# Kernel optimization log

Hardware: AMD Instinct MI355X
Metric: run time of the kernel (lower is better)

## Reference

```python
import jax, jax.numpy as jnp
import numpy as np

B, T, DI, H, L = 32, 512, 512, 512, 4  # num_layers=4 -> 1 base LSTM + 3 CALSTM layers


def setup_inputs() -> dict:
    key = jax.random.key(0)
    ks = jax.random.split(key, 4)
    s_ih = 1.0 / np.sqrt(DI)
    s_hh = 1.0 / np.sqrt(H)
    s_ca = 1.0 / np.sqrt(2 * H)
    return {
        "x": jax.random.normal(ks[0], (B, T, DI), dtype=jnp.float32),
        "w_ih": jax.random.normal(ks[1], (4 * H, DI), dtype=jnp.float32) * s_ih,
        "w_hh": jax.random.normal(ks[2], (4 * H, H), dtype=jnp.float32) * s_hh,
        "b_ih": jnp.zeros((4 * H,), jnp.float32),
        "b_hh": jnp.zeros((4 * H,), jnp.float32),
        "ca_w": jax.random.normal(ks[3], (L - 1, 5 * H, 2 * H), dtype=jnp.float32) * s_ca,
        "ca_b": jnp.zeros((L - 1, 5 * H), jnp.float32),
    }


def _stacked_lstm(x, w_ih, w_hh, b_ih, b_hh, ca_w, ca_b):
    b = x.shape[0]
    z = jnp.zeros((b, H), x.dtype)
    bias = b_ih + b_hh

    # --- layer 0: StatefulLSTM (plain LSTM cell) ---
    def base_step(carry, x_t):
        h, c = carry
        m = x_t @ w_ih.T + h @ w_hh.T + bias  # (B, 4H)
        i, f, g, o = jnp.split(m, 4, axis=1)
        c = jax.nn.sigmoid(i) * jnp.tanh(g) + jax.nn.sigmoid(f) * c
        h = jax.nn.sigmoid(o) * jnp.tanh(c)
        return (h, c), (h, c)

    _, (hs, cs) = jax.lax.scan(base_step, (z, z), jnp.swapaxes(x, 0, 1))  # (T,B,H) each

    # --- layers 1..L-1: CALSTM with fuse_type='add' ---
    for l in range(ca_w.shape[0]):
        Wl, bl = ca_w[l], ca_b[l]

        def ca_step(carry, xt, Wl=Wl, bl=bl):
            h_prev, c_prev = carry
            h_low, c_low = xt
            m = jnp.concatenate([h_low, h_prev], axis=1) @ Wl.T + bl  # (B, 5H)
            i, f_prev, f_low, u, o = jnp.split(m, 5, axis=1)
            c = (c_prev * jax.nn.sigmoid(f_prev + 1.0)
                 + c_low * jax.nn.sigmoid(f_low + 1.0)
                 + jnp.tanh(u) * jax.nn.sigmoid(i))
            h = jax.nn.sigmoid(o) * jnp.tanh(c)
            return (h, c), (h, c)

        _, (hs, cs) = jax.lax.scan(ca_step, (z, z), (hs, cs))

    hs = jnp.swapaxes(hs, 0, 1)  # (B, T, H)
    cs = jnp.swapaxes(cs, 0, 1)
    return hs, cs


def reference(x, w_ih, w_hh, b_ih, b_hh, ca_w, ca_b):
    hs, cs = _stacked_lstm(x, w_ih, w_hh, b_ih, b_hh, ca_w, ca_b)
    # ((hs, cs), hx) with hx = last step state (length=None path)
    return (hs, cs, hs[:, -1], cs[:, -1])
```

## Files before the change

### kernel.cpp

```cpp
#include <hip/hip_runtime.h>
#include <math.h>


#define TT 512
#define HH 512
#define ROWP 1032
#define W_OFF 0
#define A_OFF 82560
#define RED_OFF A_OFF
#define MF_OFF (A_OFF + 49152)
#define LDS_BYTES (A_OFF + 66048)

#define CWS_OFF 65536
#define FL_OFF  196608
#define WS_ZERO_WORDS (FL_OFF + 1024)

typedef _Float16 half8 __attribute__((ext_vector_type(8)));
typedef float f32x4 __attribute__((ext_vector_type(4)));

__global__ void zero_ws_k(unsigned* __restrict__ ws){
    int i = blockIdx.x*blockDim.x + threadIdx.x;
    for (; i < WS_ZERO_WORDS; i += gridDim.x*blockDim.x) ws[i] = 0u;
}

__device__ __forceinline__ float sigm(float v){ return 1.f/(1.f+__expf(-v)); }

__device__ __forceinline__ void poll_layer(const unsigned* fl, int L, unsigned need){
    const int i = threadIdx.x & 63;
    const unsigned* p = fl + (L*64 + i)*4;
    for (;;){
        const unsigned v = __hip_atomic_load(p, __ATOMIC_RELAXED, __HIP_MEMORY_SCOPE_AGENT);
        if (__all((int)(v >= need))) break;
        __builtin_amdgcn_s_sleep(2);
    }
}

template<int MT>
__device__ void run_loop(const float* __restrict__ x, const float* __restrict__ b_ih,
                         const float* __restrict__ b_hh, const float* __restrict__ ca_b,
                         float* __restrict__ out, float* __restrict__ ws_f,
                         char* lds, int layer, int ub)
{
    const int tid  = threadIdx.x;
    const int lane = tid & 63;
    const int wv   = tid >> 6;
    const int i16  = lane & 15, qq = lane >> 4;
    unsigned short* hws = (unsigned short*)ws_f;
    float*    cws = ws_f + CWS_OFF;
    unsigned* fl  = (unsigned*)ws_f + FL_OFF;

    const int gu = tid & 7, gb = tid >> 3, gj = ub*8 + gu;
    float bias[5] = {0,0,0,0,0};
    if (tid < 256){
        if (MT == 2){
#pragma unroll
            for (int g = 0; g < 4; ++g) bias[g] = b_ih[g*512+gj] + b_hh[g*512+gj];
        } else {
            const float* cbl = ca_b + (layer-1)*2560;
#pragma unroll
            for (int g = 0; g < 5; ++g) bias[g] = cbl[g*512+gj];
            bias[1] += 1.f; bias[2] += 1.f;
        }
    }
    if (tid == 0 && layer > 0)
        __hip_atomic_store(fl + (layer*64+ub)*4, (unsigned)layer,
                           __ATOMIC_RELAXED, __HIP_MEMORY_SCOPE_AGENT);

    for (int tau = layer; tau < TT + layer; ++tau){
        const int t = tau - layer;
        const int p = tau & 1, q = p ^ 1;

        uint4 xpk[8];
        if (MT == 2 && (tid & 127) < 64){
#pragma unroll
            for (int it = 0; it < 8; ++it){
                const int cidx = tid + it*512;
                const int b = cidx >> 7, kc = (cidx & 127) << 3;
                const float* xs = x + ((size_t)b*TT + t)*HH + kc;
                const float4 a = *(const float4*)xs;
                const float4 c = *(const float4*)(xs + 4);
                union { _Float16 h[8]; uint4 u; } pk;
                pk.h[0]=(_Float16)a.x; pk.h[1]=(_Float16)a.y;
                pk.h[2]=(_Float16)a.z; pk.h[3]=(_Float16)a.w;
                pk.h[4]=(_Float16)c.x; pk.h[5]=(_Float16)c.y;
                pk.h[6]=(_Float16)c.z; pk.h[7]=(_Float16)c.w;
                xpk[it] = pk.u;
            }
        }

        if (wv == 0)                    poll_layer(fl, layer,   (unsigned)tau);
        else if (wv == 1 && MT == 3)    poll_layer(fl, layer-1, (unsigned)tau);
        if (wv == 0) __builtin_amdgcn_fence(__ATOMIC_ACQUIRE, "agent");
        __syncthreads();

        float cpv = 0.f, clov = 0.f;
        if (tid < 256){
            cpv = cws[(layer*2+q)*16384 + gb*512 + gj];
            if (MT == 3) clov = cws[((layer-1)*2+q)*16384 + gb*512 + gj];
        }

        if (MT == 2){
            if ((tid & 127) < 64){
#pragma unroll
                for (int it = 0; it < 8; ++it){
                    const int cidx = tid + it*512;
                    const int b = cidx >> 7, kc = (cidx & 127) << 3;
                    *(uint4*)(lds + A_OFF + (size_t)(b*ROWP + kc)*2) = xpk[it];
                }
            } else {
                const unsigned short* hprev = hws + (layer*2+q)*16384;
#pragma unroll
                for (int it = 0; it < 8; ++it){
                    const int cidx = tid + it*512;
                    const int b = cidx >> 7, kc = (cidx & 127) << 3;
                    const uint4 v = *(const uint4*)(hprev + b*512 + (kc - 512));
                    *(uint4*)(lds + A_OFF + (size_t)(b*ROWP + kc)*2) = v;
                }
            }
        } else {
            const unsigned short* hlow  = hws + ((layer-1)*2+q)*16384;
            const unsigned short* hprev = hws + (layer*2+q)*16384;
#pragma unroll
            for (int it = 0; it < 8; ++it){
                const int cidx = tid + it*512;
                const int b = cidx >> 7, kc = (cidx & 127) << 3;
                const uint4 v = (kc < 512) ? *(const uint4*)(hlow  + b*512 + kc)
                                           : *(const uint4*)(hprev + b*512 + (kc - 512));
                *(uint4*)(lds + A_OFF + (size_t)(b*ROWP + kc)*2) = v;
            }
        }
        __syncthreads();

        f32x4 acc[MT][2];
#pragma unroll
        for (int mt = 0; mt < MT; ++mt){ acc[mt][0] = (f32x4){0,0,0,0}; acc[mt][1] = (f32x4){0,0,0,0}; }
#pragma unroll
        for (int s = 0; s < 4; ++s){
            const int koff = wv*128 + s*32 + qq*8;
            half8 bfrag0 = *(const half8*)(lds + A_OFF + ((0*16 + i16)*ROWP + koff)*2);
            half8 bfrag1 = *(const half8*)(lds + A_OFF + ((1*16 + i16)*ROWP + koff)*2);
#pragma unroll
            for (int mt = 0; mt < MT; ++mt){
                half8 afrag = *(const half8*)(lds + W_OFF + ((mt*16 + i16)*ROWP + koff)*2);
                acc[mt][0] = __builtin_amdgcn_mfma_f32_16x16x32_f16(afrag, bfrag0, acc[mt][0], 0, 0, 0);
                acc[mt][1] = __builtin_amdgcn_mfma_f32_16x16x32_f16(afrag, bfrag1, acc[mt][1], 0, 0, 0);
            }
        }
        __syncthreads();

#pragma unroll
        for (int mt = 0; mt < MT; ++mt)
#pragma unroll
            for (int nt = 0; nt < 2; ++nt)
#pragma unroll
                for (int r = 0; r < 4; ++r){
                    const int m = mt*16 + qq*4 + r, n = nt*16 + i16;
                    *(float*)(lds + RED_OFF + ((wv*48 + m)*32 + n)*4) = acc[mt][nt][r];
                }
        __syncthreads();

        const int rows = (MT == 2) ? 32 : 40;
        for (int o = tid; o < rows*32; o += 512){
            const int m = o >> 5, n = o & 31;
            float sm = 0.f;
#pragma unroll
            for (int kq = 0; kq < 8; ++kq)
                sm += *(float*)(lds + RED_OFF + ((kq*48 + m)*32 + n)*4);
            *(float*)(lds + MF_OFF + o*4) = sm;
        }
        __syncthreads();

        float hval = 0.f, cval = 0.f;
        if (tid < 256){
            const float* mf = (const float*)(lds + MF_OFF);
            if (MT == 2){
                const float mi  = mf[(0*8+gu)*32 + gb] + bias[0];
                const float mff = mf[(1*8+gu)*32 + gb] + bias[1];
                const float mg  = mf[(2*8+gu)*32 + gb] + bias[2];
                const float mo  = mf[(3*8+gu)*32 + gb] + bias[3];
                cval = sigm(mi)*tanhf(mg) + sigm(mff)*cpv;
                hval = sigm(mo)*tanhf(cval);
            } else {
                const float mi  = mf[(0*8+gu)*32 + gb] + bias[0];
                const float mfp = mf[(1*8+gu)*32 + gb] + bias[1];
                const float mfl = mf[(2*8+gu)*32 + gb] + bias[2];
                const float mu  = mf[(3*8+gu)*32 + gb] + bias[3];
                const float mo  = mf[(4*8+gu)*32 + gb] + bias[4];
                cval = cpv*sigm(mfp) + clov*sigm(mfl) + tanhf(mu)*sigm(mi);
                hval = sigm(mo)*tanhf(cval);
            }
        }

        if (layer < 3){
            if (wv == 0) poll_layer(fl, layer+1, (unsigned)tau);
            __syncthreads();
        }

        const float hnb = __shfl_down(hval, 1);
        if (tid < 256){
            __hip_atomic_store(&cws[(layer*2+p)*16384 + gb*512 + gj], cval,
                               __ATOMIC_RELAXED, __HIP_MEMORY_SCOPE_AGENT);
            if ((gu & 1) == 0){
                union { _Float16 h2[2]; unsigned u; } pk;
                pk.h2[0] = (_Float16)hval; pk.h2[1] = (_Float16)hnb;
                __hip_atomic_store((unsigned*)(hws + (layer*2+p)*16384 + gb*512 + gj),
                                   pk.u, __ATOMIC_RELAXED, __HIP_MEMORY_SCOPE_AGENT);
            }
        }
        asm volatile("s_waitcnt vmcnt(0)" ::: "memory");
        __syncthreads();
        if (tid == 0)
            __hip_atomic_store(fl + (layer*64+ub)*4, (unsigned)(tau + 1),
                               __ATOMIC_RELAXED, __HIP_MEMORY_SCOPE_AGENT);

        if (layer == 3 && tid < 256){
            const size_t pos = ((size_t)gb*TT + t)*HH + gj;
            out[pos]           = hval;
            out[8388608 + pos] = cval;
            if (t == TT-1){
                out[16777216 + (size_t)gb*HH + gj] = hval;
                out[16793600 + (size_t)gb*HH + gj] = cval;
            }
        }
    }
    if (tid == 0)
        __hip_atomic_store(fl + (layer*64+ub)*4, 0x7FFFFFFFu,
                           __ATOMIC_RELAXED, __HIP_MEMORY_SCOPE_AGENT);
}

__global__ __launch_bounds__(512) void persist_k(
    const float* __restrict__ x, const float* __restrict__ w_ih,
    const float* __restrict__ w_hh, const float* __restrict__ b_ih,
    const float* __restrict__ b_hh, const float* __restrict__ ca_w,
    const float* __restrict__ ca_b, float* __restrict__ out,
    float* __restrict__ ws_f)
{
    extern __shared__ char lds[];
    const int bx = blockIdx.x;
    const int layer = bx >> 6, ub = bx & 63;
    const int tid = threadIdx.x;
    const int rows = (layer == 0) ? 32 : 40;

    for (int idx = tid; idx < rows*256; idx += 512){
        const int r = idx >> 8, k4 = (idx & 255) * 4;
        const int g = r >> 3, u = r & 7;
        const int grow = g*512 + ub*8 + u;
        const float* src;
        if (layer == 0) src = (k4 < 512) ? (w_ih + (size_t)grow*512 + k4)
                                         : (w_hh + (size_t)grow*512 + (k4 - 512));
        else            src = ca_w + (size_t)(layer-1)*2560*1024 + (size_t)grow*1024 + k4;
        const float4 v = *(const float4*)src;
        union { _Float16 h[4]; uint2 u2; } pk;
        pk.h[0]=(_Float16)v.x; pk.h[1]=(_Float16)v.y;
        pk.h[2]=(_Float16)v.z; pk.h[3]=(_Float16)v.w;
        *(uint2*)(lds + W_OFF + ((size_t)(r*ROWP + k4))*2) = pk.u2;
    }
    if (layer == 0) run_loop<2>(x, b_ih, b_hh, ca_b, out, ws_f, lds, layer, ub);
    else            run_loop<3>(x, b_ih, b_hh, ca_b, out, ws_f, lds, layer, ub);
}

extern "C" void kernel_launch(void* const* d_in, const int* in_sizes, int n_in,
                              void* d_out, int out_size, void* d_ws, size_t ws_size,
                              hipStream_t stream)
{
    const float* x    = (const float*)d_in[0];
    const float* w_ih = (const float*)d_in[1];
    const float* w_hh = (const float*)d_in[2];
    const float* b_ih = (const float*)d_in[3];
    const float* b_hh = (const float*)d_in[4];
    const float* ca_w = (const float*)d_in[5];
    const float* ca_b = (const float*)d_in[6];
    float* out = (float*)d_out;
    float* ws  = (float*)d_ws;

    (void)hipFuncSetAttribute((const void*)persist_k,
                              hipFuncAttributeMaxDynamicSharedMemorySize, LDS_BYTES);
    hipLaunchKernelGGL(zero_ws_k, dim3(64), dim3(256), 0, stream, (unsigned*)ws);
    hipLaunchKernelGGL(persist_k, dim3(256), dim3(512), LDS_BYTES, stream,
                       x, w_ih, w_hh, b_ih, b_hh, ca_w, ca_b, out, ws);
}
```

Measured before the change: 3.139 ms.

## Restructure persistent LSTM pipeline with per-wave flags, triple buffering and fragment-ordered weights

Weights are stored in LDS pre-swizzled into MFMA fragment order, and B fragments are loaded straight from global memory into registers, which removes the LDS staging of activations and one barrier. The gate waves keep the cell state in registers and publish per-wave progress flags. Other waves poll only the specific producers they depend on, and a triple-buffered h/c workspace loosens the handshake with the next layer. The risks are more global memory traffic per wave and more complex flag logic that could cause deadlock or race hazards.

```diff
diff --git a/kernel.cpp b/kernel.cpp
--- a/kernel.cpp
+++ b/kernel.cpp
@@ -4,16 +4,12 @@
 
 #define TT 512
 #define HH 512
-#define ROWP 1032
-#define W_OFF 0
-#define A_OFF 82560
-#define RED_OFF A_OFF
-#define MF_OFF (A_OFF + 49152)
-#define LDS_BYTES (A_OFF + 66048)
-
-#define CWS_OFF 65536
-#define FL_OFF  196608
-#define WS_ZERO_WORDS (FL_OFF + 1024)
+
+#define CWS_OFF 98304
+#define FL_OFF  294912
+#define WS_ZERO_WORDS 299008
+
+#define LDS_BYTES 147456
 
 typedef _Float16 half8 __attribute__((ext_vector_type(8)));
 typedef float f32x4 __attribute__((ext_vector_type(4)));
@@ -25,19 +21,15 @@
 
 __device__ __forceinline__ float sigm(float v){ return 1.f/(1.f+__expf(-v)); }
 
-__device__ __forceinline__ void poll_layer(const unsigned* fl, int L, unsigned need){
-    const int i = threadIdx.x & 63;
-    const unsigned* p = fl + (L*64 + i)*4;
-    for (;;){
-        const unsigned v = __hip_atomic_load(p, __ATOMIC_RELAXED, __HIP_MEMORY_SCOPE_AGENT);
-        if (__all((int)(v >= need))) break;
-        __builtin_amdgcn_s_sleep(2);
-    }
+__device__ __forceinline__ unsigned fload(const unsigned* p){
+    return __hip_atomic_load(p, __ATOMIC_RELAXED, __HIP_MEMORY_SCOPE_AGENT);
 }
 
 template<int MT>
-__device__ void run_loop(const float* __restrict__ x, const float* __restrict__ b_ih,
-                         const float* __restrict__ b_hh, const float* __restrict__ ca_b,
+__device__ void run_loop(const float* __restrict__ x,
+                         const float* __restrict__ w_ih, const float* __restrict__ w_hh,
+                         const float* __restrict__ b_ih, const float* __restrict__ b_hh,
+                         const float* __restrict__ ca_w, const float* __restrict__ ca_b,
                          float* __restrict__ out, float* __restrict__ ws_f,
                          char* lds, int layer, int ub)
 {
@@ -45,13 +37,42 @@
     const int lane = tid & 63;
     const int wv   = tid >> 6;
     const int i16  = lane & 15, qq = lane >> 4;
+    const bool isGate = (wv >= 4);
     unsigned short* hws = (unsigned short*)ws_f;
     float*    cws = ws_f + CWS_OFF;
     unsigned* fl  = (unsigned*)ws_f + FL_OFF;
-
-    const int gu = tid & 7, gb = tid >> 3, gj = ub*8 + gu;
+    float* red = (float*)(lds + MT*32768);
+
+    for (int idx = tid; idx < MT*2048; idx += 512){
+        const int ll  = idx & 63;
+        const int s   = (idx >> 6) & 3;
+        const int wvv = (idx >> 8) & 7;
+        const int mt  = idx >> 11;
+        const int r   = mt*16 + (ll & 15);
+        const int k   = wvv*128 + s*32 + (ll >> 4)*8;
+        union { _Float16 h[8]; uint4 u; } pk;
+        if (MT == 3 && r >= 40){
+            pk.u = make_uint4(0u,0u,0u,0u);
+        } else {
+            const int g = r >> 3, u = r & 7;
+            const int grow = g*512 + ub*8 + u;
+            const float* src;
+            if (MT == 2) src = (k < 512) ? (w_ih + (size_t)grow*512 + k)
+                                         : (w_hh + (size_t)grow*512 + (k - 512));
+            else         src = ca_w + (size_t)(layer-1)*2560*1024 + (size_t)grow*1024 + k;
+            const float4 a = *(const float4*)src;
+            const float4 b = *(const float4*)(src + 4);
+            pk.h[0]=(_Float16)a.x; pk.h[1]=(_Float16)a.y; pk.h[2]=(_Float16)a.z; pk.h[3]=(_Float16)a.w;
+            pk.h[4]=(_Float16)b.x; pk.h[5]=(_Float16)b.y; pk.h[6]=(_Float16)b.z; pk.h[7]=(_Float16)b.w;
+        }
+        *(uint4*)(lds + idx*16) = pk.u;
+    }
+
+    const int gtid = tid - 256;
+    const int gu = gtid & 7, gbl = gtid >> 3;
+    const int gj = ub*8 + gu;
     float bias[5] = {0,0,0,0,0};
-    if (tid < 256){
+    if (isGate){
         if (MT == 2){
 #pragma unroll
             for (int g = 0; g < 4; ++g) bias[g] = b_ih[g*512+gj] + b_hh[g*512+gj];
@@ -62,170 +83,178 @@
             bias[1] += 1.f; bias[2] += 1.f;
         }
     }
-    if (tid == 0 && layer > 0)
-        __hip_atomic_store(fl + (layer*64+ub)*4, (unsigned)layer,
+
+    const unsigned* pollp  = nullptr;
+    const unsigned* belowp = nullptr;
+    const unsigned* warp_p = nullptr;
+    if (isGate){
+        pollp = fl + ((layer*64 + ((wv-4)*16 + (lane>>2)))*4 + (lane&3))*4;
+        if (MT == 3) belowp = fl + (((layer-1)*64 + ub)*4 + (wv-4))*4;
+    } else if (MT == 3){
+        pollp = fl + (((layer-1)*64 + (wv*16 + (lane>>2)))*4 + (lane&3))*4;
+    }
+    if (wv == 0 && layer < 3) warp_p = fl + (((layer+1)*64 + lane)*4 + 0)*4;
+
+    if (tid < 4)
+        __hip_atomic_store(fl + ((layer*64+ub)*4 + tid)*4, (unsigned)layer,
                            __ATOMIC_RELAXED, __HIP_MEMORY_SCOPE_AGENT);
+    __syncthreads();
+
+    float creg = 0.f;
 
     for (int tau = layer; tau < TT + layer; ++tau){
-        const int t = tau - layer;
-        const int p = tau & 1, q = p ^ 1;
-
-        uint4 xpk[8];
-        if (MT == 2 && (tid & 127) < 64){
-#pragma unroll
-            for (int it = 0; it < 8; ++it){
-                const int cidx = tid + it*512;
-                const int b = cidx >> 7, kc = (cidx & 127) << 3;
-                const float* xs = x + ((size_t)b*TT + t)*HH + kc;
-                const float4 a = *(const float4*)xs;
-                const float4 c = *(const float4*)(xs + 4);
-                union { _Float16 h[8]; uint4 u; } pk;
-                pk.h[0]=(_Float16)a.x; pk.h[1]=(_Float16)a.y;
-                pk.h[2]=(_Float16)a.z; pk.h[3]=(_Float16)a.w;
-                pk.h[4]=(_Float16)c.x; pk.h[5]=(_Float16)c.y;
-                pk.h[6]=(_Float16)c.z; pk.h[7]=(_Float16)c.w;
-                xpk[it] = pk.u;
-            }
-        }
-
-        if (wv == 0)                    poll_layer(fl, layer,   (unsigned)tau);
-        else if (wv == 1 && MT == 3)    poll_layer(fl, layer-1, (unsigned)tau);
-        if (wv == 0) __builtin_amdgcn_fence(__ATOMIC_ACQUIRE, "agent");
+        const int t  = tau - layer;
+        const int pb = tau % 3;
+        const int qb = (tau + 2) % 3;
+
+        if (warp_p){
+            const unsigned need = (tau >= 1) ? (unsigned)(tau - 1) : 0u;
+            for (;;){
+                if (__all((int)(fload(warp_p) >= need))) break;
+                __builtin_amdgcn_s_sleep(1);
+            }
+        }
+
+        if (MT == 3 && !isGate){
+            for (;;){
+                if (__all((int)(fload(pollp) >= (unsigned)tau))) break;
+                __builtin_amdgcn_s_sleep(1);
+            }
+            __builtin_amdgcn_fence(__ATOMIC_ACQUIRE, "agent");
+        }
+        if (isGate){
+            if (MT == 3){
+                for (;;){
+                    const unsigned v1 = fload(pollp);
+                    const unsigned v2 = fload(belowp);
+                    if (__all((int)(v1 >= (unsigned)tau && v2 >= (unsigned)tau))) break;
+                    __builtin_amdgcn_s_sleep(1);
+                }
+            } else {
+                for (;;){
+                    if (__all((int)(fload(pollp) >= (unsigned)tau))) break;
+                    __builtin_amdgcn_s_sleep(1);
+                }
+            }
+            __builtin_amdgcn_fence(__ATOMIC_ACQUIRE, "agent");
+        }
+
+        float clov = 0.f;
+        if (isGate && MT == 3)
+            clov = cws[(size_t)(((layer-1)*3 + qb)*32 + gbl)*512 + gj];
+
+        f32x4 acc[MT][2];
+#pragma unroll
+        for (int mt = 0; mt < MT; ++mt){ acc[mt][0] = (f32x4){0,0,0,0}; acc[mt][1] = (f32x4){0,0,0,0}; }
+
+        if (MT == 2 && !isGate){
+            half8 bf0[4], bf1[4];
+#pragma unroll
+            for (int s = 0; s < 4; ++s){
+                const int k = wv*128 + s*32 + qq*8;
+                const float* x0 = x + ((size_t)i16*TT + t)*HH + k;
+                const float* x1 = x + ((size_t)(16+i16)*TT + t)*HH + k;
+                const float4 a0 = *(const float4*)x0, a1 = *(const float4*)(x0+4);
+                const float4 c0 = *(const float4*)x1, c1 = *(const float4*)(x1+4);
+                half8 h0, h1;
+                h0[0]=(_Float16)a0.x; h0[1]=(_Float16)a0.y; h0[2]=(_Float16)a0.z; h0[3]=(_Float16)a0.w;
+                h0[4]=(_Float16)a1.x; h0[5]=(_Float16)a1.y; h0[6]=(_Float16)a1.z; h0[7]=(_Float16)a1.w;
+                h1[0]=(_Float16)c0.x; h1[1]=(_Float16)c0.y; h1[2]=(_Float16)c0.z; h1[3]=(_Float16)c0.w;
+                h1[4]=(_Float16)c1.x; h1[5]=(_Float16)c1.y; h1[6]=(_Float16)c1.z; h1[7]=(_Float16)c1.w;
+                bf0[s] = h0; bf1[s] = h1;
+            }
+#pragma unroll
+            for (int s = 0; s < 4; ++s)
+#pragma unroll
+                for (int mt = 0; mt < MT; ++mt){
+                    const half8 af = *(const half8*)(lds + (((mt*8 + wv)*4 + s)*64 + lane)*16);
+                    acc[mt][0] = __builtin_amdgcn_mfma_f32_16x16x32_f16(af, bf0[s], acc[mt][0], 0, 0, 0);
+                    acc[mt][1] = __builtin_amdgcn_mfma_f32_16x16x32_f16(af, bf1[s], acc[mt][1], 0, 0, 0);
+                }
+        } else {
+            const unsigned short* hsrc = isGate
+                ? hws + (size_t)((layer*3 + qb)*32)*512
+                : hws + (size_t)(((layer-1)*3 + qb)*32)*512;
+            const int kb = (wv & 3)*128;
+            half8 bf0[4], bf1[4];
+#pragma unroll
+            for (int s = 0; s < 4; ++s){
+                const int k = kb + s*32 + qq*8;
+                bf0[s] = *(const half8*)(hsrc + (size_t)i16*512 + k);
+                bf1[s] = *(const half8*)(hsrc + (size_t)(16+i16)*512 + k);
+            }
+#pragma unroll
+            for (int s = 0; s < 4; ++s)
+#pragma unroll
+                for (int mt = 0; mt < MT; ++mt){
+                    const half8 af = *(const half8*)(lds + (((mt*8 + wv)*4 + s)*64 + lane)*16);
+                    acc[mt][0] = __builtin_amdgcn_mfma_f32_16x16x32_f16(af, bf0[s], acc[mt][0], 0, 0, 0);
+                    acc[mt][1] = __builtin_amdgcn_mfma_f32_16x16x32_f16(af, bf1[s], acc[mt][1], 0, 0, 0);
+                }
+        }
+
         __syncthreads();
 
-        float cpv = 0.f, clov = 0.f;
-        if (tid < 256){
-            cpv = cws[(layer*2+q)*16384 + gb*512 + gj];
-            if (MT == 3) clov = cws[((layer-1)*2+q)*16384 + gb*512 + gj];
-        }
-
-        if (MT == 2){
-            if ((tid & 127) < 64){
-#pragma unroll
-                for (int it = 0; it < 8; ++it){
-                    const int cidx = tid + it*512;
-                    const int b = cidx >> 7, kc = (cidx & 127) << 3;
-                    *(uint4*)(lds + A_OFF + (size_t)(b*ROWP + kc)*2) = xpk[it];
-                }
+#pragma unroll
+        for (int mt = 0; mt < MT; ++mt)
+#pragma unroll
+            for (int nt = 0; nt < 2; ++nt)
+#pragma unroll
+                for (int r = 0; r < 4; ++r)
+                    red[((((wv*MT + mt)*2 + nt)*4 + r)*4 + qq)*16 + ((i16 + 4*r)&15)] = acc[mt][nt][r];
+
+        __syncthreads();
+
+        if (isGate){
+            const int NG = (MT == 2) ? 4 : 5;
+            float mg[5];
+#pragma unroll
+            for (int g = 0; g < 5; ++g){
+                if (g >= NG) break;
+                const int m = g*8 + gu, mt2 = m >> 4, mr = m & 15, q2 = mr >> 2, r2 = mr & 3;
+                const int nt2 = gbl >> 4, i2 = gbl & 15;
+                const int base = (((mt2*2 + nt2)*4 + r2)*4 + q2)*16 + ((i2 + 4*r2)&15);
+                float sm = 0.f;
+#pragma unroll
+                for (int kv = 0; kv < 8; ++kv) sm += red[base + kv*MT*512];
+                mg[g] = sm + bias[g];
+            }
+            float cval, hval;
+            if (MT == 2){
+                cval = sigm(mg[0])*tanhf(mg[2]) + sigm(mg[1])*creg;
+                hval = sigm(mg[3])*tanhf(cval);
             } else {
-                const unsigned short* hprev = hws + (layer*2+q)*16384;
-#pragma unroll
-                for (int it = 0; it < 8; ++it){
-                    const int cidx = tid + it*512;
-                    const int b = cidx >> 7, kc = (cidx & 127) << 3;
-                    const uint4 v = *(const uint4*)(hprev + b*512 + (kc - 512));
-                    *(uint4*)(lds + A_OFF + (size_t)(b*ROWP + kc)*2) = v;
-                }
-            }
-        } else {
-            const unsigned short* hlow  = hws + ((layer-1)*2+q)*16384;
-            const unsigned short* hprev = hws + (layer*2+q)*16384;
-#pragma unroll
-            for (int it = 0; it < 8; ++it){
-                const int cidx = tid + it*512;
-                const int b = cidx >> 7, kc = (cidx & 127) << 3;
-                const uint4 v = (kc < 512) ? *(const uint4*)(hlow  + b*512 + kc)
-                                           : *(const uint4*)(hprev + b*512 + (kc - 512));
-                *(uint4*)(lds + A_OFF + (size_t)(b*ROWP + kc)*2) = v;
-            }
-        }
-        __syncthreads();
-
-        f32x4 acc[MT][2];
-#pragma unroll
-        for (int mt = 0; mt < MT; ++mt){ acc[mt][0] = (f32x4){0,0,0,0}; acc[mt][1] = (f32x4){0,0,0,0}; }
-#pragma unroll
-        for (int s = 0; s < 4; ++s){
-            const int koff = wv*128 + s*32 + qq*8;
-            half8 bfrag0 = *(const half8*)(lds + A_OFF + ((0*16 + i16)*ROWP + koff)*2);
-            half8 bfrag1 = *(const half8*)(lds + A_OFF + ((1*16 + i16)*ROWP + koff)*2);
-#pragma unroll
-            for (int mt = 0; mt < MT; ++mt){
-                half8 afrag = *(const half8*)(lds + W_OFF + ((mt*16 + i16)*ROWP + koff)*2);
-                acc[mt][0] = __builtin_amdgcn_mfma_f32_16x16x32_f16(afrag, bfrag0, acc[mt][0], 0, 0, 0);
-                acc[mt][1] = __builtin_amdgcn_mfma_f32_16x16x32_f16(afrag, bfrag1, acc[mt][1], 0, 0, 0);
-            }
-        }
-        __syncthreads();
-
-#pragma unroll
-        for (int mt = 0; mt < MT; ++mt)
-#pragma unroll
-            for (int nt = 0; nt < 2; ++nt)
-#pragma unroll
-                for (int r = 0; r < 4; ++r){
-                    const int m = mt*16 + qq*4 + r, n = nt*16 + i16;
-                    *(float*)(lds + RED_OFF + ((wv*48 + m)*32 + n)*4) = acc[mt][nt][r];
-                }
-        __syncthreads();
-
-        const int rows = (MT == 2) ? 32 : 40;
-        for (int o = tid; o < rows*32; o += 512){
-            const int m = o >> 5, n = o & 31;
-            float sm = 0.f;
-#pragma unroll
-            for (int kq = 0; kq < 8; ++kq)
-                sm += *(float*)(lds + RED_OFF + ((kq*48 + m)*32 + n)*4);
-            *(float*)(lds + MF_OFF + o*4) = sm;
-        }
-        __syncthreads();
-
-        float hval = 0.f, cval = 0.f;
-        if (tid < 256){
-            const float* mf = (const float*)(lds + MF_OFF);
-            if (MT == 2){
-                const float mi  = mf[(0*8+gu)*32 + gb] + bias[0];
-                const float mff = mf[(1*8+gu)*32 + gb] + bias[1];
-                const float mg  = mf[(2*8+gu)*32 + gb] + bias[2];
-                const float mo  = mf[(3*8+gu)*32 + gb] + bias[3];
-                cval = sigm(mi)*tanhf(mg) + sigm(mff)*cpv;
-                hval = sigm(mo)*tanhf(cval);
-            } else {
-                const float mi  = mf[(0*8+gu)*32 + gb] + bias[0];
-                const float mfp = mf[(1*8+gu)*32 + gb] + bias[1];
-                const float mfl = mf[(2*8+gu)*32 + gb] + bias[2];
-                const float mu  = mf[(3*8+gu)*32 + gb] + bias[3];
-                const float mo  = mf[(4*8+gu)*32 + gb] + bias[4];
-                cval = cpv*sigm(mfp) + clov*sigm(mfl) + tanhf(mu)*sigm(mi);
-                hval = sigm(mo)*tanhf(cval);
-            }
-        }
-
-        if (layer < 3){
-            if (wv == 0) poll_layer(fl, layer+1, (unsigned)tau);
-            __syncthreads();
-        }
-
-        const float hnb = __shfl_down(hval, 1);
-        if (tid < 256){
-            __hip_atomic_store(&cws[(layer*2+p)*16384 + gb*512 + gj], cval,
-                               __ATOMIC_RELAXED, __HIP_MEMORY_SCOPE_AGENT);
+                cval = creg*sigm(mg[1]) + clov*sigm(mg[2]) + tanhf(mg[3])*sigm(mg[0]);
+                hval = sigm(mg[4])*tanhf(cval);
+            }
+            creg = cval;
+
+            const float hnb = __shfl_down(hval, 1);
+            if (layer < 3)
+                __hip_atomic_store(&cws[(size_t)((layer*3 + pb)*32 + gbl)*512 + gj], cval,
+                                   __ATOMIC_RELAXED, __HIP_MEMORY_SCOPE_AGENT);
             if ((gu & 1) == 0){
                 union { _Float16 h2[2]; unsigned u; } pk;
                 pk.h2[0] = (_Float16)hval; pk.h2[1] = (_Float16)hnb;
-                __hip_atomic_store((unsigned*)(hws + (layer*2+p)*16384 + gb*512 + gj),
+                __hip_atomic_store((unsigned*)(hws + (size_t)((layer*3 + pb)*32 + gbl)*512 + gj),
                                    pk.u, __ATOMIC_RELAXED, __HIP_MEMORY_SCOPE_AGENT);
             }
-        }
-        asm volatile("s_waitcnt vmcnt(0)" ::: "memory");
-        __syncthreads();
-        if (tid == 0)
-            __hip_atomic_store(fl + (layer*64+ub)*4, (unsigned)(tau + 1),
-                               __ATOMIC_RELAXED, __HIP_MEMORY_SCOPE_AGENT);
-
-        if (layer == 3 && tid < 256){
-            const size_t pos = ((size_t)gb*TT + t)*HH + gj;
-            out[pos]           = hval;
-            out[8388608 + pos] = cval;
-            if (t == TT-1){
-                out[16777216 + (size_t)gb*HH + gj] = hval;
-                out[16793600 + (size_t)gb*HH + gj] = cval;
-            }
-        }
-    }
-    if (tid == 0)
-        __hip_atomic_store(fl + (layer*64+ub)*4, 0x7FFFFFFFu,
-                           __ATOMIC_RELAXED, __HIP_MEMORY_SCOPE_AGENT);
+            asm volatile("s_waitcnt vmcnt(0)" ::: "memory");
+            if (lane == 0)
+                __hip_atomic_store(fl + ((layer*64 + ub)*4 + (wv-4))*4, (unsigned)(tau + 1),
+                                   __ATOMIC_RELAXED, __HIP_MEMORY_SCOPE_AGENT);
+
+            if (MT == 3 && layer == 3){
+                const size_t pos = ((size_t)gbl*TT + t)*HH + gj;
+                out[pos]           = hval;
+                out[8388608 + pos] = cval;
+                if (t == TT-1){
+                    out[16777216 + (size_t)gbl*HH + gj] = hval;
+                    out[16793600 + (size_t)gbl*HH + gj] = cval;
+                }
+            }
+        }
+    }
 }
 
 __global__ __launch_bounds__(512) void persist_k(
@@ -238,25 +267,8 @@
     extern __shared__ char lds[];
     const int bx = blockIdx.x;
     const int layer = bx >> 6, ub = bx & 63;
-    const int tid = threadIdx.x;
-    const int rows = (layer == 0) ? 32 : 40;
-
-    for (int idx = tid; idx < rows*256; idx += 512){
-        const int r = idx >> 8, k4 = (idx & 255) * 4;
-        const int g = r >> 3, u = r & 7;
-        const int grow = g*512 + ub*8 + u;
-        const float* src;
-        if (layer == 0) src = (k4 < 512) ? (w_ih + (size_t)grow*512 + k4)
-                                         : (w_hh + (size_t)grow*512 + (k4 - 512));
-        else            src = ca_w + (size_t)(layer-1)*2560*1024 + (size_t)grow*1024 + k4;
-        const float4 v = *(const float4*)src;
-        union { _Float16 h[4]; uint2 u2; } pk;
-        pk.h[0]=(_Float16)v.x; pk.h[1]=(_Float16)v.y;
-        pk.h[2]=(_Float16)v.z; pk.h[3]=(_Float16)v.w;
-        *(uint2*)(lds + W_OFF + ((size_t)(r*ROWP + k4))*2) = pk.u2;
-    }
-    if (layer == 0) run_loop<2>(x, b_ih, b_hh, ca_b, out, ws_f, lds, layer, ub);
-    else            run_loop<3>(x, b_ih, b_hh, ca_b, out, ws_f, lds, layer, ub);
+    if (layer == 0) run_loop<2>(x, w_ih, w_hh, b_ih, b_hh, ca_w, ca_b, out, ws_f, lds, layer, ub);
+    else            run_loop<3>(x, w_ih, w_hh, b_ih, b_hh, ca_w, ca_b, out, ws_f, lds, layer, ub);
 }
 
 extern "C" void kernel_launch(void* const* d_in, const int* in_sizes, int n_in,
```

Result: slower. 8.577 ms (+173.3%).

## Triple-buffer layer state, fuse reduction into gate math, keep cell state in registers

Applied to the files above, without the earlier changes.

Switches the inter-layer h/c workspace from double to triple buffering. This lets the wait on the next layer move to the start of the step, handled by a separate wave, with a one-step lag instead of a mid-step poll and extra barrier. The cross-wave K-reduction now happens directly in the gate threads from a swizzled layout, which removes the intermediate MF buffer pass and one __syncthreads. The layer's own cell state is carried in a register instead of being reloaded from global memory, and the last layer no longer writes c to the workspace. The cost is more workspace memory and more complex indexing.

```diff
diff --git a/kernel.cpp b/kernel.cpp
--- a/kernel.cpp
+++ b/kernel.cpp
@@ -8,11 +8,10 @@
 #define W_OFF 0
 #define A_OFF 82560
 #define RED_OFF A_OFF
-#define MF_OFF (A_OFF + 49152)
 #define LDS_BYTES (A_OFF + 66048)
 
-#define CWS_OFF 65536
-#define FL_OFF  196608
+#define CWS_OFF 98304
+#define FL_OFF  294912
 #define WS_ZERO_WORDS (FL_OFF + 1024)
 
 typedef _Float16 half8 __attribute__((ext_vector_type(8)));
@@ -48,6 +47,7 @@
     unsigned short* hws = (unsigned short*)ws_f;
     float*    cws = ws_f + CWS_OFF;
     unsigned* fl  = (unsigned*)ws_f + FL_OFF;
+    float* red = (float*)(lds + RED_OFF);
 
     const int gu = tid & 7, gb = tid >> 3, gj = ub*8 + gu;
     float bias[5] = {0,0,0,0,0};
@@ -66,9 +66,12 @@
         __hip_atomic_store(fl + (layer*64+ub)*4, (unsigned)layer,
                            __ATOMIC_RELAXED, __HIP_MEMORY_SCOPE_AGENT);
 
+    float creg = 0.f;
+
     for (int tau = layer; tau < TT + layer; ++tau){
-        const int t = tau - layer;
-        const int p = tau & 1, q = p ^ 1;
+        const int t  = tau - layer;
+        const int pb = tau % 3;
+        const int qb = (tau + 2) % 3;
 
         uint4 xpk[8];
         if (MT == 2 && (tid & 127) < 64){
@@ -90,14 +93,14 @@
 
         if (wv == 0)                    poll_layer(fl, layer,   (unsigned)tau);
         else if (wv == 1 && MT == 3)    poll_layer(fl, layer-1, (unsigned)tau);
+        else if (wv == 2 && layer < 3)  poll_layer(fl, layer+1,
+                                            (tau > 0) ? (unsigned)(tau-1) : 0u);
         if (wv == 0) __builtin_amdgcn_fence(__ATOMIC_ACQUIRE, "agent");
         __syncthreads();
 
-        float cpv = 0.f, clov = 0.f;
-        if (tid < 256){
-            cpv = cws[(layer*2+q)*16384 + gb*512 + gj];
-            if (MT == 3) clov = cws[((layer-1)*2+q)*16384 + gb*512 + gj];
-        }
+        float clov = 0.f;
+        if (MT == 3 && tid < 256)
+            clov = cws[((layer-1)*3+qb)*16384 + gb*512 + gj];
 
         if (MT == 2){
             if ((tid & 127) < 64){
@@ -108,7 +111,7 @@
                     *(uint4*)(lds + A_OFF + (size_t)(b*ROWP + kc)*2) = xpk[it];
                 }
             } else {
-                const unsigned short* hprev = hws + (layer*2+q)*16384;
+                const unsigned short* hprev = hws + (layer*3+qb)*16384;
 #pragma unroll
                 for (int it = 0; it < 8; ++it){
                     const int cidx = tid + it*512;
@@ -118,8 +121,8 @@
                 }
             }
         } else {
-            const unsigned short* hlow  = hws + ((layer-1)*2+q)*16384;
-            const unsigned short* hprev = hws + (layer*2+q)*16384;
+            const unsigned short* hlow  = hws + ((layer-1)*3+qb)*16384;
+            const unsigned short* hprev = hws + (layer*3+qb)*16384;
 #pragma unroll
             for (int it = 0; it < 8; ++it){
                 const int cidx = tid + it*512;
@@ -153,57 +156,43 @@
 #pragma unroll
             for (int nt = 0; nt < 2; ++nt)
 #pragma unroll
-                for (int r = 0; r < 4; ++r){
-                    const int m = mt*16 + qq*4 + r, n = nt*16 + i16;
-                    *(float*)(lds + RED_OFF + ((wv*48 + m)*32 + n)*4) = acc[mt][nt][r];
-                }
-        __syncthreads();
-
-        const int rows = (MT == 2) ? 32 : 40;
-        for (int o = tid; o < rows*32; o += 512){
-            const int m = o >> 5, n = o & 31;
-            float sm = 0.f;
-#pragma unroll
-            for (int kq = 0; kq < 8; ++kq)
-                sm += *(float*)(lds + RED_OFF + ((kq*48 + m)*32 + n)*4);
-            *(float*)(lds + MF_OFF + o*4) = sm;
-        }
+                for (int r = 0; r < 4; ++r)
+                    red[((((wv*MT + mt)*2 + nt)*4 + r)*4 + qq)*16 + ((i16 + 4*r)&15)] = acc[mt][nt][r];
         __syncthreads();
 
         float hval = 0.f, cval = 0.f;
         if (tid < 256){
-            const float* mf = (const float*)(lds + MF_OFF);
+            const int NG = (MT == 2) ? 4 : 5;
+            float mg[5];
+#pragma unroll
+            for (int g = 0; g < NG; ++g){
+                const int m = g*8 + gu, mt2 = m >> 4, mr = m & 15, q2 = mr >> 2, r2 = mr & 3;
+                const int nt2 = gb >> 4, i2 = gb & 15;
+                const int base = (((mt2*2 + nt2)*4 + r2)*4 + q2)*16 + ((i2 + 4*r2)&15);
+                float sm = 0.f;
+#pragma unroll
+                for (int kv = 0; kv < 8; ++kv) sm += red[base + kv*MT*512];
+                mg[g] = sm + bias[g];
+            }
             if (MT == 2){
-                const float mi  = mf[(0*8+gu)*32 + gb] + bias[0];
-                const float mff = mf[(1*8+gu)*32 + gb] + bias[1];
-                const float mg  = mf[(2*8+gu)*32 + gb] + bias[2];
-                const float mo  = mf[(3*8+gu)*32 + gb] + bias[3];
-                cval = sigm(mi)*tanhf(mg) + sigm(mff)*cpv;
-                hval = sigm(mo)*tanhf(cval);
+                cval = sigm(mg[0])*tanhf(mg[2]) + sigm(mg[1])*creg;
+                hval = sigm(mg[3])*tanhf(cval);
             } else {
-                const float mi  = mf[(0*8+gu)*32 + gb] + bias[0];
-                const float mfp = mf[(1*8+gu)*32 + gb] + bias[1];
-                const float mfl = mf[(2*8+gu)*32 + gb] + bias[2];
-                const float mu  = mf[(3*8+gu)*32 + gb] + bias[3];
-                const float mo  = mf[(4*8+gu)*32 + gb] + bias[4];
-                cval = cpv*sigm(mfp) + clov*sigm(mfl) + tanhf(mu)*sigm(mi);
-                hval = sigm(mo)*tanhf(cval);
-            }
-        }
-
-        if (layer < 3){
-            if (wv == 0) poll_layer(fl, layer+1, (unsigned)tau);
-            __syncthreads();
+                cval = creg*sigm(mg[1]) + clov*sigm(mg[2]) + tanhf(mg[3])*sigm(mg[0]);
+                hval = sigm(mg[4])*tanhf(cval);
+            }
+            creg = cval;
         }
 
         const float hnb = __shfl_down(hval, 1);
         if (tid < 256){
-            __hip_atomic_store(&cws[(layer*2+p)*16384 + gb*512 + gj], cval,
-                               __ATOMIC_RELAXED, __HIP_MEMORY_SCOPE_AGENT);
+            if (layer < 3)
+                __hip_atomic_store(&cws[(layer*3+pb)*16384 + gb*512 + gj], cval,
+                                   __ATOMIC_RELAXED, __HIP_MEMORY_SCOPE_AGENT);
             if ((gu & 1) == 0){
                 union { _Float16 h2[2]; unsigned u; } pk;
                 pk.h2[0] = (_Float16)hval; pk.h2[1] = (_Float16)hnb;
-                __hip_atomic_store((unsigned*)(hws + (layer*2+p)*16384 + gb*512 + gj),
+                __hip_atomic_store((unsigned*)(hws + (layer*3+pb)*16384 + gb*512 + gj),
                                    pk.u, __ATOMIC_RELAXED, __HIP_MEMORY_SCOPE_AGENT);
             }
         }
```

Result: no change. 3.157 ms (+0.6%).
